# Kernel tuning notes

Hardware: AMD Instinct MI355X
Metric: run time of the kernel (lower is better)

Reference implementation:

```python
import jax, jax.numpy as jnp
import numpy as np


def _log_g(x):
    # log of g(x) = where(x>=0, x+0.5, sigmoid(x)), computed stably in log space
    return jnp.where(x >= 0.0, jnp.log(jax.nn.relu(x) + 0.5), -jax.nn.softplus(-x))


def setup_inputs() -> dict:
    key = jax.random.key(0)
    k1, k2, k3, k4 = jax.random.split(key, 4)
    B, T, D, H = 4, 8192, 512, 512
    x = jax.random.normal(k1, (B, T, D), dtype=jnp.float32)
    h_prev = jax.random.uniform(k2, (B, 1, H), dtype=jnp.float32)  # positive: log(h0) taken
    W_h = jax.random.normal(k3, (H, D), dtype=jnp.float32) * (1.0 / np.sqrt(D))
    b_h = jnp.zeros((H,), dtype=jnp.float32)
    W_z = jax.random.normal(k4, (H, D), dtype=jnp.float32) * (1.0 / np.sqrt(D))
    b_z = jnp.zeros((H,), dtype=jnp.float32)
    return {"x": x, "h_prev": h_prev, "W_h": W_h, "b_h": b_h, "W_z": W_z, "b_z": b_z}


def reference(x, h_prev, W_h, b_h, W_z, b_z):
    # parallel (seq_len > 1) minGRU forward via Heinsen log-space scan
    k = jnp.einsum('btd,hd->bth', x, W_z) + b_z           # (B,T,H) gate pre-activation
    log_z = -jax.nn.softplus(-k)                          # log sigmoid(k)
    log_coeffs = -jax.nn.softplus(k)                      # log (1 - sigmoid(k))
    log_tilde_h = _log_g(jnp.einsum('btd,hd->bth', x, W_h) + b_h)
    log_h0 = jnp.log(h_prev)                              # (B,1,H)
    log_values = jnp.concatenate([log_h0, log_z + log_tilde_h], axis=1)  # (B,T+1,H)
    # a_star = [0, cumsum(log_coeffs)]
    a_star = jnp.pad(jnp.cumsum(log_coeffs, axis=1), ((0, 0), (1, 0), (0, 0)))
    log_h = a_star + jax.lax.cumlogsumexp(log_values - a_star, axis=1)
    h = jnp.exp(log_h)[:, 1:]                             # drop h0 -> (B,T,H)
    return h
```

## Files before the change

kernel.cpp:

```cpp
#include <hip/hip_runtime.h>
#include <hip/hip_bf16.h>
#include <stdint.h>

#define B_ 4
#define T_ 8192
#define D_ 512
#define H_ 512
#define M_ (B_ * T_)
#define SEG 32
#define NSEG (M_ / SEG)

typedef __attribute__((ext_vector_type(8))) short short8;
typedef __attribute__((ext_vector_type(4))) float floatx4;

__device__ __forceinline__ unsigned short f2bf(float f) {
    union { float f; unsigned int u; } v; v.f = f;
    unsigned int u = v.u;
    u += 0x7fffu + ((u >> 16) & 1u);
    return (unsigned short)(u >> 16);
}
__device__ __forceinline__ float bf_lo(unsigned int u) {
    union { unsigned int i; float f; } a; a.i = u << 16; return a.f;
}
__device__ __forceinline__ float bf_hi(unsigned int u) {
    union { unsigned int i; float f; } a; a.i = u & 0xffff0000u; return a.f;
}
__device__ __forceinline__ unsigned int pk_cd(float c, float d) {
    return (unsigned int)f2bf(c) | ((unsigned int)f2bf(d) << 16);
}

__global__ void conv_all(const float* __restrict__ x,
                         const float* __restrict__ Wz,
                         const float* __restrict__ Wh,
                         unsigned short* __restrict__ xbf,
                         unsigned short* __restrict__ Wf)
{
    const int X4 = M_ * D_ / 4;
    const int W4 = H_ * D_ / 4;
    int i = blockIdx.x * blockDim.x + threadIdx.x;
    const float* src; unsigned short* dst; int idx;
    if (i < X4)             { src = x;  dst = xbf;                  idx = i; }
    else if (i < X4 + W4)   { src = Wz; dst = Wf;                   idx = i - X4; }
    else if (i < X4 + 2*W4) { src = Wh; dst = Wf + (size_t)H_ * D_; idx = i - X4 - W4; }
    else return;
    float4 v = ((const float4*)src)[idx];
    ushort4 w; w.x = f2bf(v.x); w.y = f2bf(v.y); w.z = f2bf(v.z); w.w = f2bf(v.w);
    ((ushort4*)dst)[idx] = w;
}

#define LDSB 35840

__global__ __launch_bounds__(256, 3)
void gemm_cd(const unsigned short* __restrict__ xbf,
             const unsigned short* __restrict__ Wf,
             const float* __restrict__ bz, const float* __restrict__ bh,
             unsigned int* __restrict__ cd,
             float2* __restrict__ Sagg)
{
    __shared__ __align__(16) char smem[LDSB];
    unsigned short* lds = (unsigned short*)smem;
    unsigned int*   cdl = (unsigned int*)smem;

    const int tid  = threadIdx.x;
    const int lane = tid & 63;
    const int wave = tid >> 6;
    const int xcd  = blockIdx.x & 7;
    const int nblk = (blockIdx.x >> 3) & 7;
    const int mblk = xcd * 32 + (blockIdx.x >> 6);
    const int m0 = mblk * 128;
    const int n0 = nblk * 64;
    const int wm = (wave >> 1) * 64;
    const int wn = (wave & 1) * 32;
    const int l15  = lane & 15;
    const int quad = lane >> 4;
    const int srow = lane >> 2;
    const int sp   = lane & 3;

    #define STAGE(p, kt)                                                          \
    {                                                                             \
        const int kb = (kt) * 32;                                                 \
        unsigned short* bb = lds + (p) * 8192;                                    \
        _Pragma("unroll")                                                         \
        for (int r = 0; r < 2; ++r) {                                             \
            const int chunk = r * 4 + wave;                                       \
            const int row   = chunk * 16 + srow;                                  \
            const int kp    = sp ^ (row & 3);                                     \
            __builtin_amdgcn_global_load_lds(                                     \
                (const __attribute__((address_space(1))) unsigned int*)           \
                    (xbf + (size_t)(m0 + row) * D_ + kb + kp * 8),                \
                (__attribute__((address_space(3))) unsigned int*)(bb + chunk * 512),\
                16, 0, 0);                                                        \
        }                                                                         \
        {                                                                         \
            const int row = wave * 16 + srow;                                     \
            const int kp  = sp ^ (row & 3);                                       \
            __builtin_amdgcn_global_load_lds(                                     \
                (const __attribute__((address_space(1))) unsigned int*)           \
                    (Wf + (size_t)(n0 + row) * D_ + kb + kp * 8),                 \
                (__attribute__((address_space(3))) unsigned int*)(bb + 4096 + wave * 512),\
                16, 0, 0);                                                        \
            __builtin_amdgcn_global_load_lds(                                     \
                (const __attribute__((address_space(1))) unsigned int*)           \
                    (Wf + (size_t)(512 + n0 + row) * D_ + kb + kp * 8),           \
                (__attribute__((address_space(3))) unsigned int*)(bb + 6144 + wave * 512),\
                16, 0, 0);                                                        \
        }                                                                         \
    }

    floatx4 acc_z[4][2], acc_h[4][2];
    #pragma unroll
    for (int i = 0; i < 4; ++i)
        #pragma unroll
        for (int j = 0; j < 2; ++j) { acc_z[i][j] = (floatx4)0.0f; acc_h[i][j] = (floatx4)0.0f; }

    STAGE(0, 0);

    for (int kt = 0; kt < 16; ++kt) {
        __syncthreads();
        const int base = (kt & 1) * 8192;
        short8 af[4], zf[2], hf[2];
        #pragma unroll
        for (int i = 0; i < 4; ++i) {
            const int ra = wm + i * 16 + l15;
            af[i] = *(const short8*)&lds[base + ra * 32 + ((quad ^ (ra & 3)) * 8)];
        }
        #pragma unroll
        for (int j = 0; j < 2; ++j) {
            const int rb = wn + j * 16 + l15;
            zf[j] = *(const short8*)&lds[base + 4096 + rb * 32 + ((quad ^ (rb & 3)) * 8)];
            hf[j] = *(const short8*)&lds[base + 6144 + rb * 32 + ((quad ^ (rb & 3)) * 8)];
        }
        if (kt < 15) STAGE((kt + 1) & 1, kt + 1);
        #pragma unroll
        for (int i = 0; i < 4; ++i)
            #pragma unroll
            for (int j = 0; j < 2; ++j) {
                acc_z[i][j] = __builtin_amdgcn_mfma_f32_16x16x32_bf16(zf[j], af[i], acc_z[i][j], 0, 0, 0);
                acc_h[i][j] = __builtin_amdgcn_mfma_f32_16x16x32_bf16(hf[j], af[i], acc_h[i][j], 0, 0, 0);
            }
    }

    __syncthreads();

    #pragma unroll
    for (int j = 0; j < 2; ++j) {
        const int hlb = wn + j * 16 + quad * 4;
        const float4 bzv = *(const float4*)&bz[n0 + hlb];
        const float4 bhv = *(const float4*)&bh[n0 + hlb];
        #pragma unroll
        for (int i = 0; i < 4; ++i) {
            const int mloc = wm + i * 16 + l15;
            uint4 w;
            #pragma unroll
            for (int r = 0; r < 4; ++r) {
                float kz = acc_z[i][j][r] + ((const float*)&bzv)[r];
                float hp = acc_h[i][j][r] + ((const float*)&bhv)[r];
                float c  = 1.0f / (1.0f + __expf(kz));
                float g  = (hp >= 0.0f) ? (hp + 0.5f) : (1.0f / (1.0f + __expf(-hp)));
                float d  = (1.0f - c) * g;
                ((unsigned int*)&w)[r] = pk_cd(c, d);
            }
            *(uint4*)&cd[(size_t)(m0 + mloc) * H_ + n0 + hlb] = w;
            *(uint4*)&cdl[mloc * 68 + hlb] = w;
        }
    }

    __syncthreads();

    {
        float C = 1.0f, Dv = 0.0f;
        const int t0 = wave * 32;
        #pragma unroll
        for (int t = 0; t < 32; ++t) {
            unsigned int u = cdl[(t0 + t) * 68 + lane];
            float c = bf_lo(u), d = bf_hi(u);
            Dv = fmaf(c, Dv, d);
            C *= c;
        }
        Sagg[(size_t)((m0 >> 5) + wave) * H_ + n0 + lane] = make_float2(C, Dv);
    }
    #undef STAGE
}

__global__ __launch_bounds__(256)
void interseg(const float* __restrict__ h_prev,
              const float2* __restrict__ Sagg,
              float* __restrict__ Hseg)
{
    const int flat = blockIdx.x * 256 + threadIdx.x;
    const int b = flat >> 9;
    const int h = flat & 511;
    float hs = h_prev[(size_t)b * H_ + h];
    #pragma unroll 8
    for (int s = 0; s < T_ / SEG; ++s) {
        size_t o = (size_t)(b * (T_ / SEG) + s) * H_ + h;
        Hseg[o] = hs;
        float2 cdv = Sagg[o];
        hs = fmaf(cdv.x, hs, cdv.y);
    }
}

__global__ __launch_bounds__(256)
void apply_scan(const unsigned int* __restrict__ cd,
                const float* __restrict__ Hseg,
                float* __restrict__ out)
{
    const int sg   = blockIdx.x >> 1;
    const int half = blockIdx.x & 1;
    const int h = half * 256 + threadIdx.x;
    float hs = Hseg[(size_t)sg * H_ + h];
    const unsigned int* base = cd + (size_t)sg * SEG * H_ + h;
    float* ob = out + (size_t)sg * SEG * H_ + h;
    #pragma unroll 8
    for (int t = 0; t < SEG; ++t) {
        unsigned int u = base[(size_t)t * H_];
        hs = fmaf(bf_lo(u), hs, bf_hi(u));
        ob[(size_t)t * H_] = hs;
    }
}

extern "C" void kernel_launch(void* const* d_in, const int* in_sizes, int n_in,
                              void* d_out, int out_size, void* d_ws, size_t ws_size,
                              hipStream_t stream)
{
    const float* x      = (const float*)d_in[0];
    const float* h_prev = (const float*)d_in[1];
    const float* W_h    = (const float*)d_in[2];
    const float* b_h    = (const float*)d_in[3];
    const float* W_z    = (const float*)d_in[4];
    const float* b_z    = (const float*)d_in[5];
    float* out = (float*)d_out;

    unsigned short* xbf = (unsigned short*)d_out;

    char* ws = (char*)d_ws;
    unsigned int* cd = (unsigned int*)ws;
    size_t cd_bytes = (size_t)M_ * H_ * 4;
    unsigned short* Wf = (unsigned short*)(ws + cd_bytes);
    size_t wf_bytes = (size_t)2 * H_ * D_ * sizeof(unsigned short);
    float2* Sagg = (float2*)(ws + cd_bytes + wf_bytes);
    float*  Hseg = (float*)(ws + cd_bytes + wf_bytes + (size_t)NSEG * H_ * sizeof(float2));

    {
        int total = M_ * D_ / 4 + 2 * (H_ * D_ / 4);
        conv_all<<<dim3((total + 255) / 256), dim3(256), 0, stream>>>(x, W_z, W_h, xbf, Wf);
    }
    gemm_cd<<<dim3((M_ / 128) * (H_ / 64)), dim3(256), 0, stream>>>(
        xbf, Wf, b_z, b_h, cd, Sagg);
    interseg<<<dim3(8), dim3(256), 0, stream>>>(h_prev, Sagg, Hseg);
    apply_scan<<<dim3(NSEG * 2), dim3(256), 0, stream>>>(cd, Hseg, out);
}
```

Before: 213.8 us.

## Parallelize inter-segment scan with wave shuffles and transpose segment aggregate layout

The serial inter-segment scan used only 8 blocks, each walking 256 segments in order. It now runs one wave per (batch,h) chain, with each lane combining 4 segments and a shuffle-based prefix scan across the wave, launched over 512 blocks. Sagg and Hseg are transposed to chain-major so each lane reads contiguously. apply_scan now handles two channels per thread with nontemporal 8-byte loads and stores, which halves its block count, but its Hseg reads become strided.

```diff
diff --git a/kernel.cpp b/kernel.cpp
--- a/kernel.cpp
+++ b/kernel.cpp
@@ -8,10 +8,13 @@
 #define H_ 512
 #define M_ (B_ * T_)
 #define SEG 32
+#define SPB 256
 #define NSEG (M_ / SEG)
 
 typedef __attribute__((ext_vector_type(8))) short short8;
 typedef __attribute__((ext_vector_type(4))) float floatx4;
+typedef __attribute__((ext_vector_type(2))) unsigned int uint2e;
+typedef __attribute__((ext_vector_type(2))) float float2e;
 
 __device__ __forceinline__ unsigned short f2bf(float f) {
     union { float f; unsigned int u; } v; v.f = f;
@@ -177,7 +180,9 @@
             Dv = fmaf(c, Dv, d);
             C *= c;
         }
-        Sagg[(size_t)((m0 >> 5) + wave) * H_ + n0 + lane] = make_float2(C, Dv);
+        const int chain = (m0 >> 13) * 512 + n0 + lane;
+        const int seg   = ((m0 >> 5) & 255) + wave;
+        Sagg[(size_t)chain * SPB + seg] = make_float2(C, Dv);
     }
     #undef STAGE
 }
@@ -187,17 +192,32 @@
               const float2* __restrict__ Sagg,
               float* __restrict__ Hseg)
 {
-    const int flat = blockIdx.x * 256 + threadIdx.x;
-    const int b = flat >> 9;
-    const int h = flat & 511;
-    float hs = h_prev[(size_t)b * H_ + h];
-    #pragma unroll 8
-    for (int s = 0; s < T_ / SEG; ++s) {
-        size_t o = (size_t)(b * (T_ / SEG) + s) * H_ + h;
-        Hseg[o] = hs;
-        float2 cdv = Sagg[o];
-        hs = fmaf(cdv.x, hs, cdv.y);
-    }
+    const int chain = blockIdx.x * 4 + (threadIdx.x >> 6);
+    const int lane  = threadIdx.x & 63;
+    const float2* spp = Sagg + (size_t)chain * SPB + lane * 4;
+    float4 q0 = *(const float4*)&spp[0];
+    float4 q1 = *(const float4*)&spp[2];
+    float C = q0.x, D = q0.y;
+    D = fmaf(q0.z, D, q0.w);  C *= q0.z;
+    D = fmaf(q1.x, D, q1.y);  C *= q1.x;
+    D = fmaf(q1.z, D, q1.w);  C *= q1.z;
+    #pragma unroll
+    for (int off = 1; off < 64; off <<= 1) {
+        float Cp = __shfl_up(C, off, 64);
+        float Dp = __shfl_up(D, off, 64);
+        if (lane >= off) { D = fmaf(C, Dp, D); C *= Cp; }
+    }
+    float Ce = __shfl_up(C, 1, 64);
+    float De = __shfl_up(D, 1, 64);
+    if (lane == 0) { Ce = 1.0f; De = 0.0f; }
+    const float h0 = h_prev[chain];
+    float hs = fmaf(Ce, h0, De);
+    float4 o;
+    o.x = hs;
+    hs = fmaf(q0.x, hs, q0.y); o.y = hs;
+    hs = fmaf(q0.z, hs, q0.w); o.z = hs;
+    hs = fmaf(q1.x, hs, q1.y); o.w = hs;
+    *(float4*)&Hseg[(size_t)chain * SPB + lane * 4] = o;
 }
 
 __global__ __launch_bounds__(256)
@@ -205,17 +225,21 @@
                 const float* __restrict__ Hseg,
                 float* __restrict__ out)
 {
-    const int sg   = blockIdx.x >> 1;
-    const int half = blockIdx.x & 1;
-    const int h = half * 256 + threadIdx.x;
-    float hs = Hseg[(size_t)sg * H_ + h];
+    const int sg = blockIdx.x;
+    const int b  = sg >> 8;
+    const int s  = sg & 255;
+    const int h  = threadIdx.x * 2;
+    float hs0 = Hseg[(size_t)(b * 512 + h)     * SPB + s];
+    float hs1 = Hseg[(size_t)(b * 512 + h + 1) * SPB + s];
     const unsigned int* base = cd + (size_t)sg * SEG * H_ + h;
     float* ob = out + (size_t)sg * SEG * H_ + h;
-    #pragma unroll 8
+    #pragma unroll
     for (int t = 0; t < SEG; ++t) {
-        unsigned int u = base[(size_t)t * H_];
-        hs = fmaf(bf_lo(u), hs, bf_hi(u));
-        ob[(size_t)t * H_] = hs;
+        uint2e v = __builtin_nontemporal_load((const uint2e*)(base + (size_t)t * H_));
+        hs0 = fmaf(bf_lo(v.x), hs0, bf_hi(v.x));
+        hs1 = fmaf(bf_lo(v.y), hs1, bf_hi(v.y));
+        float2e o; o.x = hs0; o.y = hs1;
+        __builtin_nontemporal_store(o, (float2e*)(ob + (size_t)t * H_));
     }
 }
 
@@ -239,7 +263,7 @@
     unsigned short* Wf = (unsigned short*)(ws + cd_bytes);
     size_t wf_bytes = (size_t)2 * H_ * D_ * sizeof(unsigned short);
     float2* Sagg = (float2*)(ws + cd_bytes + wf_bytes);
-    float*  Hseg = (float*)(ws + cd_bytes + wf_bytes + (size_t)NSEG * H_ * sizeof(float2));
+    float*  Hseg = (float*)((char*)Sagg + (size_t)2048 * SPB * sizeof(float2));
 
     {
         int total = M_ * D_ / 4 + 2 * (H_ * D_ / 4);
@@ -247,6 +271,6 @@
     }
     gemm_cd<<<dim3((M_ / 128) * (H_ / 64)), dim3(256), 0, stream>>>(
         xbf, Wf, b_z, b_h, cd, Sagg);
-    interseg<<<dim3(8), dim3(256), 0, stream>>>(h_prev, Sagg, Hseg);
-    apply_scan<<<dim3(NSEG * 2), dim3(256), 0, stream>>>(cd, Hseg, out);
-}
+    interseg<<<dim3(512), dim3(256), 0, stream>>>(h_prev, Sagg, Hseg);
+    apply_scan<<<dim3(NSEG), dim3(256), 0, stream>>>(cd, Hseg, out);
+}
```

New measurement: 192.9 us. 9.8% less time.
